# Optimization experiments

Measured on AMD Instinct MI355X. Metric: run time of the kernel, lower is better.

The kernel has to match this reference:

```python
import jax, jax.numpy as jnp
import numpy as np

N = 100000   # num_nodes
E = 1600000  # num_edges
DIN = 128
H1 = 256
H2 = 128
SLOPE = 0.01  # torch leaky_relu default negative slope


def _gcn_conv(h, W, b, src, dst):
    # GCNConv: add self-loops, symmetric deg^-1/2 normalization, linear transform, scatter-add, bias
    hw = h @ W  # [N, out]
    loops = jnp.arange(N)
    s = jnp.concatenate([src, loops])
    d = jnp.concatenate([dst, loops])
    deg = jax.ops.segment_sum(jnp.ones(s.shape[0], dtype=hw.dtype), d, num_segments=N)
    dis = jnp.where(deg > 0, jax.lax.rsqrt(deg), 0.0)
    msg = hw[s] * (dis[s] * dis[d])[:, None]
    return jax.ops.segment_sum(msg, d, num_segments=N) + b


def _gru_cell(x, h, Wih, Whh, bih, bhh):
    # torch.nn.GRUCell semantics; weight layout [3H, in], gate order r, z, n
    gi = x @ Wih.T + bih
    gh = h @ Whh.T + bhh
    ir, iz, inn = jnp.split(gi, 3, axis=-1)
    hr, hz, hn = jnp.split(gh, 3, axis=-1)
    r = jax.nn.sigmoid(ir + hr)
    z = jax.nn.sigmoid(iz + hz)
    n = jnp.tanh(inn + r * hn)
    return (1.0 - z) * n + z * h


def setup_inputs() -> dict:
    key = jax.random.key(0)
    ks = jax.random.split(key, 24)
    rn = lambda k, shape, s=0.05: (jax.random.normal(k, shape) * s).astype(jnp.float32)
    return {
        "x": rn(ks[0], (N, DIN), 1.0),
        "edge_index": jax.random.randint(ks[1], (2, E), 0, N, dtype=jnp.int32),
        "prev0": rn(ks[2], (N, H1), 1.0),
        "prev1": rn(ks[3], (N, H2), 1.0),
        "Wp1": rn(ks[4], (DIN, 256)), "bp1": jnp.zeros((256,), jnp.float32),
        "Wp2": rn(ks[5], (256, 128)), "bp2": jnp.zeros((128,), jnp.float32),
        "Wc1": rn(ks[6], (128, H1)), "bc1": jnp.zeros((H1,), jnp.float32),
        "Wc2": rn(ks[7], (H1, H2)), "bc2": jnp.zeros((H2,), jnp.float32),
        "Wih1": rn(ks[8], (3 * H1, H1)), "Whh1": rn(ks[9], (3 * H1, H1)),
        "bih1": jnp.zeros((3 * H1,), jnp.float32), "bhh1": jnp.zeros((3 * H1,), jnp.float32),
        "Wih2": rn(ks[10], (3 * H2, H2)), "Whh2": rn(ks[11], (3 * H2, H2)),
        "bih2": jnp.zeros((3 * H2,), jnp.float32), "bhh2": jnp.zeros((3 * H2,), jnp.float32),
        "Wpost": rn(ks[12], (H2, 2)), "bpost": jnp.zeros((2,), jnp.float32),
    }


def reference(x, edge_index, prev0, prev1, Wp1, bp1, Wp2, bp2, Wc1, bc1, Wc2, bc2,
              Wih1, Whh1, bih1, bhh1, Wih2, Whh2, bih2, bhh2, Wpost, bpost):
    src, dst = edge_index[0], edge_index[1]
    # preprocess MLP (dropout p=0 => identity)
    h = jax.nn.leaky_relu(x @ Wp1 + bp1, SLOPE)
    h = jax.nn.leaky_relu(h @ Wp2 + bp2, SLOPE)
    # GCN layer 1 + GRU temporal update
    h = jax.nn.leaky_relu(_gcn_conv(h, Wc1, bc1, src, dst), SLOPE)
    h = _gru_cell(h, prev0, Wih1, Whh1, bih1, bhh1)
    emb0 = h
    # GCN layer 2 + GRU temporal update
    h = jax.nn.leaky_relu(_gcn_conv(h, Wc2, bc2, src, dst), SLOPE)
    h = _gru_cell(h, prev1, Wih2, Whh2, bih2, bhh2)
    emb1 = h
    # postprocess and reduce
    out = jnp.sum(h @ Wpost + bpost, axis=-1)  # [N]
    return out, emb0, emb1
```

## Files before the change

### kernel.cpp

```cpp
#include <hip/hip_runtime.h>
#include <cstdint>
#include <cstddef>

typedef __bf16 bf16x8 __attribute__((ext_vector_type(8)));
typedef float f32x4 __attribute__((ext_vector_type(4)));
typedef unsigned short us16;

__device__ __forceinline__ float lrelu(float v) { return v >= 0.0f ? v : 0.01f * v; }
__device__ __forceinline__ float fsigmoid(float x) {
  x = fminf(fmaxf(x, -30.0f), 30.0f);
  return 1.0f / (1.0f + __expf(-x));
}
__device__ __forceinline__ float ftanh(float x) {
  x = fminf(fmaxf(x, -15.0f), 15.0f);
  float e = __expf(2.0f * x);
  return (e - 1.0f) / (e + 1.0f);
}
__device__ __forceinline__ us16 f2b(float f) {
  unsigned int u = __builtin_bit_cast(unsigned int, f);
  u = (u + 0x7fffu + ((u >> 16) & 1u)) >> 16;
  return (us16)u;
}
__device__ __forceinline__ float b2f(us16 h) {
  unsigned int u = ((unsigned int)h) << 16;
  return __builtin_bit_cast(float, u);
}
__device__ __forceinline__ unsigned pk2(float a, float b) {
  return (unsigned)f2b(a) | ((unsigned)f2b(b) << 16);
}
__device__ __forceinline__ void unp8(int4 v, float* t) {
  unsigned a = (unsigned)v.x, b = (unsigned)v.y, c = (unsigned)v.z, d = (unsigned)v.w;
  t[0] = b2f((us16)(a & 0xffff)); t[1] = b2f((us16)(a >> 16));
  t[2] = b2f((us16)(b & 0xffff)); t[3] = b2f((us16)(b >> 16));
  t[4] = b2f((us16)(c & 0xffff)); t[5] = b2f((us16)(c >> 16));
  t[6] = b2f((us16)(d & 0xffff)); t[7] = b2f((us16)(d >> 16));
}

__device__ __forceinline__ void stage16(const us16* gsrc, us16* ldst) {
  __builtin_amdgcn_global_load_lds(
      (const __attribute__((address_space(1))) unsigned int*)(const void*)gsrc,
      (__attribute__((address_space(3))) unsigned int*)(void*)ldst, 16, 0, 0);
}
__device__ __forceinline__ bf16x8 frag_rd(const us16* base, int row, int byte_in_row) {
  int byte = row * 128 + (byte_in_row ^ ((row & 7) << 4));
  return *(const bf16x8*)((const char*)base + byte);
}

__global__ void k_deg(const int* __restrict__ dst, int* __restrict__ indeg, int E) {
  int e = blockIdx.x * 256 + threadIdx.x;
  if (e < E) atomicAdd(&indeg[dst[e]], 1);
}

__global__ void k_dis(const int* __restrict__ indeg, float* __restrict__ dis, int n) {
  int i = blockIdx.x * 256 + threadIdx.x;
  if (i < n) dis[i] = rsqrtf((float)(indeg[i] + 1));
}

__global__ __launch_bounds__(1024) void k_scan1(const int* __restrict__ v, int* __restrict__ rp,
                                                int* __restrict__ part, int n) {
  __shared__ int wsum[16];
  int base = blockIdx.x << 10;
  int t = threadIdx.x, lane = t & 63, wv = t >> 6;
  int val = (base + t < n) ? v[base + t] : 0;
  int s = val;
  #pragma unroll
  for (int off = 1; off < 64; off <<= 1) {
    int u = __shfl_up(s, off);
    if (lane >= off) s += u;
  }
  if (lane == 63) wsum[wv] = s;
  __syncthreads();
  int wadd = 0;
  #pragma unroll
  for (int w = 0; w < 16; ++w) wadd += (w < wv) ? wsum[w] : 0;
  if (base + t < n) rp[base + t] = wadd + s - val;
  if (t == 0) {
    int tot = 0;
    #pragma unroll
    for (int w = 0; w < 16; ++w) tot += wsum[w];
    part[blockIdx.x] = tot;
  }
}

__global__ __launch_bounds__(1024) void k_scan2(int* __restrict__ p, int nc) {
  __shared__ int wsum[16];
  int t = threadIdx.x, lane = t & 63, wv = t >> 6;
  int val = (t < nc) ? p[t] : 0;
  int s = val;
  #pragma unroll
  for (int off = 1; off < 64; off <<= 1) {
    int u = __shfl_up(s, off);
    if (lane >= off) s += u;
  }
  if (lane == 63) wsum[wv] = s;
  __syncthreads();
  int wadd = 0;
  #pragma unroll
  for (int w = 0; w < 16; ++w) wadd += (w < wv) ? wsum[w] : 0;
  if (t < nc) p[t] = wadd + s - val;
}

__global__ void k_scan3(int* __restrict__ rp, const int* __restrict__ part, int n, int total) {
  int i = blockIdx.x * 256 + threadIdx.x;
  if (i < n) rp[i] += part[i >> 10];
  else if (i == n) rp[n] = total;
}

__global__ void k_fill(const int* __restrict__ src, const int* __restrict__ dst,
                       const float* __restrict__ dis, int* __restrict__ cursor,
                       int* __restrict__ csrc, float* __restrict__ cw, int E) {
  int e = blockIdx.x * 256 + threadIdx.x;
  if (e >= E) return;
  int s = src[e], d = dst[e];
  int pos = atomicAdd(&cursor[d], 1);
  csrc[pos] = s;
  cw[pos] = dis[s] * dis[d];
}

__global__ void k_cast(const float* __restrict__ in, us16* __restrict__ out, int n) {
  int i = (blockIdx.x * 256 + threadIdx.x) * 4;
  if (i >= n) return;
  float4 v = *(const float4*)(in + i);
  *(ushort4*)(out + i) = make_ushort4(f2b(v.x), f2b(v.y), f2b(v.z), f2b(v.w));
}

__global__ void k_tpose(const float* __restrict__ in, us16* __restrict__ out, int R, int C) {
  int t = blockIdx.x * 256 + threadIdx.x;
  if (t >= R * C) return;
  int r = t % R, c = t / R;
  out[(size_t)c * R + r] = f2b(in[(size_t)r * C + c]);
}

template<int ACT, int BIAS>
__global__ __launch_bounds__(256) void k_mm(const us16* __restrict__ A,
                                            const us16* __restrict__ Bt,
                                            const float* __restrict__ bias,
                                            us16* __restrict__ Cb,
                                            int M, int K, int Nc, int ny) {
  __shared__ __align__(16) us16 As[128 * 64];
  __shared__ __align__(16) us16 Bs[128 * 64];
  const int bm = (blockIdx.x / ny) * 128;
  const int bn = (blockIdx.x % ny) * 128;
  const int tid = threadIdx.x;
  const int lane = tid & 63;
  const int wave = tid >> 6;
  const int wm = (wave >> 1) * 64;
  const int wn = (wave & 1) * 64;
  const int lr = lane & 15;
  const int lk = lane >> 4;
  const int srow = lane >> 3;
  const int schk = (lane & 7) ^ srow;
  f32x4 acc[4][4] = {};
  for (int k0 = 0; k0 < K; k0 += 64) {
    #pragma unroll
    for (int it = 0; it < 4; ++it) {
      int r8 = (wave * 4 + it) * 8;
      int ar = bm + r8 + srow; if (ar >= M) ar = M - 1;
      stage16(A + (size_t)ar * K + k0 + schk * 8, As + r8 * 64);
      stage16(Bt + (size_t)(bn + r8 + srow) * K + k0 + schk * 8, Bs + r8 * 64);
    }
    __syncthreads();
    #pragma unroll
    for (int kk = 0; kk < 2; ++kk) {
      bf16x8 af[4], bq[4];
      #pragma unroll
      for (int i = 0; i < 4; ++i) af[i] = frag_rd(As, wm + i * 16 + lr, kk * 64 + lk * 16);
      #pragma unroll
      for (int j = 0; j < 4; ++j) bq[j] = frag_rd(Bs, wn + j * 16 + lr, kk * 64 + lk * 16);
      #pragma unroll
      for (int i = 0; i < 4; ++i)
        #pragma unroll
        for (int j = 0; j < 4; ++j)
          acc[i][j] = __builtin_amdgcn_mfma_f32_16x16x32_bf16(af[i], bq[j], acc[i][j], 0, 0, 0);
    }
    __syncthreads();
  }
  float bb[4];
  #pragma unroll
  for (int j = 0; j < 4; ++j) bb[j] = BIAS ? bias[bn + wn + j * 16 + lr] : 0.0f;
  #pragma unroll
  for (int i = 0; i < 4; ++i) {
    #pragma unroll
    for (int q = 0; q < 4; ++q) {
      int row = bm + wm + i * 16 + lk * 4 + q;
      if (row < M) {
        #pragma unroll
        for (int j = 0; j < 4; ++j) {
          int col = bn + wn + j * 16 + lr;
          float v = acc[i][j][q] + bb[j];
          if (ACT) v = lrelu(v);
          Cb[(size_t)row * Nc + col] = f2b(v);
        }
      }
    }
  }
}

template<int ACT>
__global__ __launch_bounds__(256) void k_agg128(const us16* __restrict__ hw, const int* __restrict__ rp,
                                                const int* __restrict__ csrc, const float* __restrict__ cw,
                                                const float* __restrict__ dis, const float* __restrict__ bias,
                                                us16* __restrict__ outp, int M) {
  int node = blockIdx.x * 16 + (threadIdx.x >> 4);
  int l = threadIdx.x & 15;
  if (node >= M) return;
  const us16* base = hw + l * 8;
  float acc[8], t0[8], t1[8], t2[8], t3[8];
  float dn = dis[node];
  float sw = dn * dn;
  {
    int4 v = *(const int4*)(base + (size_t)node * 128);
    unp8(v, t0);
    #pragma unroll
    for (int j = 0; j < 8; ++j) acc[j] = t0[j] * sw;
  }
  int e = rp[node], e1 = rp[node + 1];
  for (; e + 4 <= e1; e += 4) {
    int s0 = csrc[e], s1 = csrc[e + 1], s2 = csrc[e + 2], s3 = csrc[e + 3];
    float w0 = cw[e], w1 = cw[e + 1], w2 = cw[e + 2], w3 = cw[e + 3];
    int4 v0 = *(const int4*)(base + (size_t)s0 * 128);
    int4 v1 = *(const int4*)(base + (size_t)s1 * 128);
    int4 v2 = *(const int4*)(base + (size_t)s2 * 128);
    int4 v3 = *(const int4*)(base + (size_t)s3 * 128);
    unp8(v0, t0); unp8(v1, t1); unp8(v2, t2); unp8(v3, t3);
    #pragma unroll
    for (int j = 0; j < 8; ++j) acc[j] = fmaf(w0, t0[j], acc[j]);
    #pragma unroll
    for (int j = 0; j < 8; ++j) acc[j] = fmaf(w1, t1[j], acc[j]);
    #pragma unroll
    for (int j = 0; j < 8; ++j) acc[j] = fmaf(w2, t2[j], acc[j]);
    #pragma unroll
    for (int j = 0; j < 8; ++j) acc[j] = fmaf(w3, t3[j], acc[j]);
  }
  for (; e < e1; ++e) {
    int s0 = csrc[e];
    float w0 = cw[e];
    int4 v0 = *(const int4*)(base + (size_t)s0 * 128);
    unp8(v0, t0);
    #pragma unroll
    for (int j = 0; j < 8; ++j) acc[j] = fmaf(w0, t0[j], acc[j]);
  }
  if (ACT) {
    float4 b0 = *(const float4*)(bias + l * 8);
    float4 b1 = *(const float4*)(bias + l * 8 + 4);
    float bb[8] = {b0.x, b0.y, b0.z, b0.w, b1.x, b1.y, b1.z, b1.w};
    #pragma unroll
    for (int j = 0; j < 8; ++j) acc[j] = lrelu(acc[j] + bb[j]);
  }
  int4 o;
  o.x = (int)pk2(acc[0], acc[1]);
  o.y = (int)pk2(acc[2], acc[3]);
  o.z = (int)pk2(acc[4], acc[5]);
  o.w = (int)pk2(acc[6], acc[7]);
  *(int4*)(outp + (size_t)node * 128 + l * 8) = o;
}

template<int H, int WB>
__global__ __launch_bounds__(256) void k_fgru(const us16* __restrict__ xb, const us16* __restrict__ hb,
                                              const us16* __restrict__ Wih, const us16* __restrict__ Whh,
                                              const float* __restrict__ bih, const float* __restrict__ bhh,
                                              float* __restrict__ emb, us16* __restrict__ embb,
                                              int M, int ny) {
  __shared__ __align__(16) us16 as_[128 * 64];
  __shared__ __align__(16) us16 ws[3 * 64 * 64];
  const int bn = (blockIdx.x % ny) * 64;
  const int bm = (blockIdx.x / ny) * 128;
  const int tid = threadIdx.x;
  const int lane = tid & 63, wave = tid >> 6;
  const int wm = (wave >> 1) * 64, wn = (wave & 1) * 32;
  const int lr = lane & 15, lk = lane >> 4;
  const int srow = lane >> 3;
  const int schk = (lane & 7) ^ srow;

  f32x4 acc[3][4][2];
  #pragma unroll
  for (int g = 0; g < 3; ++g)
    #pragma unroll
    for (int i = 0; i < 4; ++i)
      #pragma unroll
      for (int j = 0; j < 2; ++j) acc[g][i][j] = {0.f, 0.f, 0.f, 0.f};

  for (int k0 = 0; k0 < H; k0 += 64) {
    #pragma unroll
    for (int it = 0; it < 4; ++it) {
      int r8 = (wave * 4 + it) * 8;
      int ar = bm + r8 + srow; if (ar >= M) ar = M - 1;
      stage16(xb + (size_t)ar * H + k0 + schk * 8, as_ + r8 * 64);
    }
    #pragma unroll
    for (int it = 0; it < 6; ++it) {
      int idx = wave * 6 + it;
      int g = idx >> 3, rr = (idx & 7) * 8;
      stage16(Wih + (size_t)(g * H + bn + rr + srow) * H + k0 + schk * 8,
              ws + g * 64 * 64 + rr * 64);
    }
    __syncthreads();
    #pragma unroll
    for (int kk = 0; kk < 2; ++kk) {
      bf16x8 a[4], bq[3][2];
      #pragma unroll
      for (int i = 0; i < 4; ++i) a[i] = frag_rd(as_, wm + i * 16 + lr, kk * 64 + lk * 16);
      #pragma unroll
      for (int g = 0; g < 3; ++g)
        #pragma unroll
        for (int j = 0; j < 2; ++j)
          bq[g][j] = frag_rd(ws + g * 64 * 64, wn + j * 16 + lr, kk * 64 + lk * 16);
      #pragma unroll
      for (int g = 0; g < 3; ++g)
        #pragma unroll
        for (int i = 0; i < 4; ++i)
          #pragma unroll
          for (int j = 0; j < 2; ++j)
            acc[g][i][j] = __builtin_amdgcn_mfma_f32_16x16x32_bf16(a[i], bq[g][j], acc[g][i][j], 0, 0, 0);
    }
    __syncthreads();
  }
  uint2 pgi[3][4][2];
  #pragma unroll
  for (int g = 0; g < 3; ++g)
    #pragma unroll
    for (int i = 0; i < 4; ++i)
      #pragma unroll
      for (int j = 0; j < 2; ++j) {
        pgi[g][i][j].x = pk2(acc[g][i][j][0], acc[g][i][j][1]);
        pgi[g][i][j].y = pk2(acc[g][i][j][2], acc[g][i][j][3]);
        acc[g][i][j] = {0.f, 0.f, 0.f, 0.f};
      }
  for (int k0 = 0; k0 < H; k0 += 64) {
    #pragma unroll
    for (int it = 0; it < 4; ++it) {
      int r8 = (wave * 4 + it) * 8;
      int ar = bm + r8 + srow; if (ar >= M) ar = M - 1;
      stage16(hb + (size_t)ar * H + k0 + schk * 8, as_ + r8 * 64);
    }
    #pragma unroll
    for (int it = 0; it < 6; ++it) {
      int idx = wave * 6 + it;
      int g = idx >> 3, rr = (idx & 7) * 8;
      stage16(Whh + (size_t)(g * H + bn + rr + srow) * H + k0 + schk * 8,
              ws + g * 64 * 64 + rr * 64);
    }
    __syncthreads();
    #pragma unroll
    for (int kk = 0; kk < 2; ++kk) {
      bf16x8 a[4], bq[3][2];
      #pragma unroll
      for (int i = 0; i < 4; ++i) a[i] = frag_rd(as_, wm + i * 16 + lr, kk * 64 + lk * 16);
      #pragma unroll
      for (int g = 0; g < 3; ++g)
        #pragma unroll
        for (int j = 0; j < 2; ++j)
          bq[g][j] = frag_rd(ws + g * 64 * 64, wn + j * 16 + lr, kk * 64 + lk * 16);
      #pragma unroll
      for (int g = 0; g < 3; ++g)
        #pragma unroll
        for (int i = 0; i < 4; ++i)
          #pragma unroll
          for (int j = 0; j < 2; ++j)
            acc[g][i][j] = __builtin_amdgcn_mfma_f32_16x16x32_bf16(a[i], bq[g][j], acc[g][i][j], 0, 0, 0);
    }
    __syncthreads();
  }
  #pragma unroll
  for (int j = 0; j < 2; ++j) {
    int col = bn + wn + j * 16 + lr;
    float sr = bih[col] + bhh[col];
    float sz = bih[H + col] + bhh[H + col];
    float bni = bih[2 * H + col];
    float bnh = bhh[2 * H + col];
    #pragma unroll
    for (int i = 0; i < 4; ++i) {
      #pragma unroll
      for (int q = 0; q < 4; ++q) {
        int row = bm + wm + i * 16 + lk * 4 + q;
        if (row >= M) continue;
        unsigned w0 = (q & 2) ? pgi[0][i][j].y : pgi[0][i][j].x;
        unsigned w1 = (q & 2) ? pgi[1][i][j].y : pgi[1][i][j].x;
        unsigned w2 = (q & 2) ? pgi[2][i][j].y : pgi[2][i][j].x;
        int sh = (q & 1) * 16;
        float gir = b2f((us16)(w0 >> sh));
        float giz = b2f((us16)(w1 >> sh));
        float gin = b2f((us16)(w2 >> sh));
        float r = fsigmoid(gir + acc[0][i][j][q] + sr);
        float z = fsigmoid(giz + acc[1][i][j][q] + sz);
        float n = ftanh(gin + bni + r * (acc[2][i][j][q] + bnh));
        float hv = b2f(hb[(size_t)row * H + col]);
        float o = (1.0f - z) * n + z * hv;
        emb[(size_t)row * H + col] = o;
        if (WB) embb[(size_t)row * H + col] = f2b(o);
      }
    }
  }
}

__global__ __launch_bounds__(256) void k_post(const float* __restrict__ emb, const float* __restrict__ Wpost,
                                              const float* __restrict__ bpost, float* __restrict__ outv, int M) {
  int gw = (int)((blockIdx.x * 256 + threadIdx.x) >> 6);
  int lane = threadIdx.x & 63;
  if (gw >= M) return;
  float2 ev = *(const float2*)(emb + (size_t)gw * 128 + lane * 2);
  float4 wv = *(const float4*)(Wpost + lane * 4);
  float p = ev.x * (wv.x + wv.y) + ev.y * (wv.z + wv.w);
  #pragma unroll
  for (int o = 32; o > 0; o >>= 1) p += __shfl_xor(p, o);
  if (lane == 0) outv[gw] = p + bpost[0] + bpost[1];
}

extern "C" void kernel_launch(void* const* d_in, const int* in_sizes, int n_in,
                              void* d_out, int out_size, void* d_ws, size_t ws_size,
                              hipStream_t stream) {
  const float* x     = (const float*)d_in[0];
  const int*   ei    = (const int*)d_in[1];
  const float* prev0 = (const float*)d_in[2];
  const float* prev1 = (const float*)d_in[3];
  const float* Wp1   = (const float*)d_in[4];
  const float* bp1   = (const float*)d_in[5];
  const float* Wp2   = (const float*)d_in[6];
  const float* bp2   = (const float*)d_in[7];
  const float* Wc1   = (const float*)d_in[8];
  const float* bc1   = (const float*)d_in[9];
  const float* Wc2   = (const float*)d_in[10];
  const float* bc2   = (const float*)d_in[11];
  const float* Wih1  = (const float*)d_in[12];
  const float* Whh1  = (const float*)d_in[13];
  const float* bih1  = (const float*)d_in[14];
  const float* bhh1  = (const float*)d_in[15];
  const float* Wih2  = (const float*)d_in[16];
  const float* Whh2  = (const float*)d_in[17];
  const float* bih2  = (const float*)d_in[18];
  const float* bhh2  = (const float*)d_in[19];
  const float* Wpost = (const float*)d_in[20];
  const float* bpost = (const float*)d_in[21];

  const int N = in_sizes[0] / 128;
  const int E = in_sizes[1] / 2;
  const int* srcp = ei;
  const int* dstp = ei + E;

  char* wsb = (char*)d_ws;
  size_t off = 0;
  auto alloc = [&](size_t bytes) -> void* {
    void* p = wsb + off;
    off = (off + bytes + 255) & ~(size_t)255;
    return p;
  };
  float* dis    = (float*)alloc((size_t)N * 4);
  int*   indeg  = (int*)alloc((size_t)N * 4);
  int*   rp     = (int*)alloc((size_t)(N + 1) * 4);
  int*   part   = (int*)alloc((size_t)1024 * 4);
  int*   cursor = (int*)alloc((size_t)N * 4);
  int*   csrc   = (int*)alloc((size_t)E * 4);
  float* cw     = (float*)alloc((size_t)E * 4);
  us16* xb    = (us16*)alloc((size_t)N * 128 * 2);
  us16* p0b   = (us16*)alloc((size_t)N * 256 * 2);
  us16* p1b   = (us16*)alloc((size_t)N * 128 * 2);
  us16* WtP1  = (us16*)alloc((size_t)256 * 128 * 2);
  us16* WtP2  = (us16*)alloc((size_t)128 * 256 * 2);
  us16* WtC1  = (us16*)alloc((size_t)256 * 128 * 2);
  us16* WtC2  = (us16*)alloc((size_t)128 * 256 * 2);
  us16* Wih1b = (us16*)alloc((size_t)768 * 256 * 2);
  us16* Whh1b = (us16*)alloc((size_t)768 * 256 * 2);
  us16* Wih2b = (us16*)alloc((size_t)384 * 128 * 2);
  us16* Whh2b = (us16*)alloc((size_t)384 * 128 * 2);
  us16* bufA  = (us16*)alloc((size_t)N * 256 * 2);
  us16* bufB  = (us16*)alloc((size_t)N * 128 * 2);
  us16* bufD  = (us16*)alloc((size_t)N * 128 * 2);
  us16* emb0b = (us16*)alloc((size_t)N * 256 * 2);
  (void)ws_size; (void)n_in; (void)out_size;

  float* outv = (float*)d_out;
  float* emb0 = outv + N;
  float* emb1 = emb0 + (size_t)N * 256;

  auto cg = [](long n) { return (unsigned)((n / 4 + 255) / 256); };

  k_cast<<<cg((long)N * 128), 256, 0, stream>>>(x, xb, N * 128);
  k_cast<<<cg((long)N * 256), 256, 0, stream>>>(prev0, p0b, N * 256);
  k_cast<<<cg((long)N * 128), 256, 0, stream>>>(prev1, p1b, N * 128);
  k_cast<<<cg(768 * 256), 256, 0, stream>>>(Wih1, Wih1b, 768 * 256);
  k_cast<<<cg(768 * 256), 256, 0, stream>>>(Whh1, Whh1b, 768 * 256);
  k_cast<<<cg(384 * 128), 256, 0, stream>>>(Wih2, Wih2b, 384 * 128);
  k_cast<<<cg(384 * 128), 256, 0, stream>>>(Whh2, Whh2b, 384 * 128);
  k_tpose<<<(128 * 256 + 255) / 256, 256, 0, stream>>>(Wp1, WtP1, 128, 256);
  k_tpose<<<(256 * 128 + 255) / 256, 256, 0, stream>>>(Wp2, WtP2, 256, 128);
  k_tpose<<<(128 * 256 + 255) / 256, 256, 0, stream>>>(Wc1, WtC1, 128, 256);
  k_tpose<<<(256 * 128 + 255) / 256, 256, 0, stream>>>(Wc2, WtC2, 256, 128);

  hipMemsetAsync(indeg, 0, (size_t)N * 4, stream);
  k_deg<<<(E + 255) / 256, 256, 0, stream>>>(dstp, indeg, E);
  k_dis<<<(N + 255) / 256, 256, 0, stream>>>(indeg, dis, N);
  const int NC = (N + 1023) / 1024;
  k_scan1<<<NC, 1024, 0, stream>>>(indeg, rp, part, N);
  k_scan2<<<1, 1024, 0, stream>>>(part, NC);
  k_scan3<<<(N + 256) / 256, 256, 0, stream>>>(rp, part, N, E);
  hipMemcpyAsync(cursor, rp, (size_t)N * 4, hipMemcpyDeviceToDevice, stream);
  k_fill<<<(E + 255) / 256, 256, 0, stream>>>(srcp, dstp, dis, cursor, csrc, cw, E);

  const int MB = (N + 127) / 128;
  const int AB = (N + 15) / 16;

  k_mm<1, 1><<<MB * 2, 256, 0, stream>>>(xb, WtP1, bp1, bufA, N, 128, 256, 2);
  k_mm<1, 1><<<MB, 256, 0, stream>>>(bufA, WtP2, bp2, bufB, N, 256, 128, 1);
  k_agg128<0><<<AB, 256, 0, stream>>>(bufB, rp, csrc, cw, dis, nullptr, bufD, N);
  k_mm<1, 1><<<MB * 2, 256, 0, stream>>>(bufD, WtC1, bc1, bufA, N, 128, 256, 2);
  k_fgru<256, 1><<<MB * 4, 256, 0, stream>>>(bufA, p0b, Wih1b, Whh1b, bih1, bhh1,
                                             emb0, emb0b, N, 4);
  k_mm<0, 0><<<MB, 256, 0, stream>>>(emb0b, WtC2, nullptr, bufB, N, 256, 128, 1);
  k_agg128<1><<<AB, 256, 0, stream>>>(bufB, rp, csrc, cw, dis, bc2, bufD, N);
  k_fgru<128, 0><<<MB * 2, 256, 0, stream>>>(bufD, p1b, Wih2b, Whh2b, bih2, bhh2,
                                             emb1, nullptr, N, 2);
  k_post<<<(N + 3) / 4, 256, 0, stream>>>(emb1, Wpost, bpost, outv, N);
}
```

Baseline: 896.7 us.

## Double-buffer LDS in GEMM and fuse GRU input/hidden GEMMs into one pipelined loop

The matmul kernel now double-buffers its LDS tiles, so the next K-slice is staged while MFMAs run on the current one, and one barrier per step is dropped. The GRU kernel is restructured to compute the input and hidden gate GEMMs together in a single K loop over 32-wide slices. It uses a 64-row tile, its own double-buffered staging and a new swizzle, and keeps six fp32 accumulator sets instead of packing the input-gate results to bf16. This removes the serial second pass, the bf16 round-trip of gi and the exposed load latency. In exchange it doubles LDS use and launches more, smaller blocks, which may cost occupancy.

```diff
diff --git a/kernel.cpp b/kernel.cpp
--- a/kernel.cpp
+++ b/kernel.cpp
@@ -44,6 +44,10 @@
 __device__ __forceinline__ bf16x8 frag_rd(const us16* base, int row, int byte_in_row) {
   int byte = row * 128 + (byte_in_row ^ ((row & 7) << 4));
   return *(const bf16x8*)((const char*)base + byte);
+}
+__device__ __forceinline__ bf16x8 frd32(const us16* tilebase, int row, int ck16) {
+  int slot = ck16 ^ ((row >> 1) & 3);
+  return *(const bf16x8*)(tilebase + row * 32 + slot * 8);
 }
 
 __global__ void k_deg(const int* __restrict__ dst, int* __restrict__ indeg, int E) {
@@ -137,8 +141,7 @@
                                             const float* __restrict__ bias,
                                             us16* __restrict__ Cb,
                                             int M, int K, int Nc, int ny) {
-  __shared__ __align__(16) us16 As[128 * 64];
-  __shared__ __align__(16) us16 Bs[128 * 64];
+  __shared__ __align__(16) us16 lds[2][2 * 8192];
   const int bm = (blockIdx.x / ny) * 128;
   const int bn = (blockIdx.x % ny) * 128;
   const int tid = threadIdx.x;
@@ -151,29 +154,36 @@
   const int srow = lane >> 3;
   const int schk = (lane & 7) ^ srow;
   f32x4 acc[4][4] = {};
-  for (int k0 = 0; k0 < K; k0 += 64) {
+
+  auto stage = [&](int k0, us16* buf) {
     #pragma unroll
     for (int it = 0; it < 4; ++it) {
       int r8 = (wave * 4 + it) * 8;
       int ar = bm + r8 + srow; if (ar >= M) ar = M - 1;
-      stage16(A + (size_t)ar * K + k0 + schk * 8, As + r8 * 64);
-      stage16(Bt + (size_t)(bn + r8 + srow) * K + k0 + schk * 8, Bs + r8 * 64);
-    }
+      stage16(A + (size_t)ar * K + k0 + schk * 8, buf + r8 * 64);
+      stage16(Bt + (size_t)(bn + r8 + srow) * K + k0 + schk * 8, buf + 8192 + r8 * 64);
+    }
+  };
+
+  const int nk = K >> 6;
+  stage(0, lds[0]);
+  for (int t = 0; t < nk; ++t) {
+    us16* cur = lds[t & 1];
     __syncthreads();
+    if (t + 1 < nk) stage((t + 1) << 6, lds[(t + 1) & 1]);
     #pragma unroll
     for (int kk = 0; kk < 2; ++kk) {
       bf16x8 af[4], bq[4];
       #pragma unroll
-      for (int i = 0; i < 4; ++i) af[i] = frag_rd(As, wm + i * 16 + lr, kk * 64 + lk * 16);
-      #pragma unroll
-      for (int j = 0; j < 4; ++j) bq[j] = frag_rd(Bs, wn + j * 16 + lr, kk * 64 + lk * 16);
+      for (int i = 0; i < 4; ++i) af[i] = frag_rd(cur, wm + i * 16 + lr, kk * 64 + lk * 16);
+      #pragma unroll
+      for (int j = 0; j < 4; ++j) bq[j] = frag_rd(cur + 8192, wn + j * 16 + lr, kk * 64 + lk * 16);
       #pragma unroll
       for (int i = 0; i < 4; ++i)
         #pragma unroll
         for (int j = 0; j < 4; ++j)
           acc[i][j] = __builtin_amdgcn_mfma_f32_16x16x32_bf16(af[i], bq[j], acc[i][j], 0, 0, 0);
     }
-    __syncthreads();
   }
   float bb[4];
   #pragma unroll
@@ -261,129 +271,91 @@
                                               const float* __restrict__ bih, const float* __restrict__ bhh,
                                               float* __restrict__ emb, us16* __restrict__ embb,
                                               int M, int ny) {
-  __shared__ __align__(16) us16 as_[128 * 64];
-  __shared__ __align__(16) us16 ws[3 * 64 * 64];
+  __shared__ __align__(16) us16 lds[2][8 * 2048];
   const int bn = (blockIdx.x % ny) * 64;
-  const int bm = (blockIdx.x / ny) * 128;
+  const int bm = (blockIdx.x / ny) * 64;
   const int tid = threadIdx.x;
   const int lane = tid & 63, wave = tid >> 6;
-  const int wm = (wave >> 1) * 64, wn = (wave & 1) * 32;
+  const int wm = (wave >> 1) * 32, wn = (wave & 1) * 32;
   const int lr = lane & 15, lk = lane >> 4;
-  const int srow = lane >> 3;
-  const int schk = (lane & 7) ^ srow;
-
-  f32x4 acc[3][4][2];
-  #pragma unroll
-  for (int g = 0; g < 3; ++g)
-    #pragma unroll
-    for (int i = 0; i < 4; ++i)
+  const int sl_row = lane >> 2;
+  const int sl_chk = (lane & 3) ^ ((lane >> 3) & 3);
+
+  f32x4 acc[6][2][2];
+  #pragma unroll
+  for (int g = 0; g < 6; ++g)
+    #pragma unroll
+    for (int i = 0; i < 2; ++i)
       #pragma unroll
       for (int j = 0; j < 2; ++j) acc[g][i][j] = {0.f, 0.f, 0.f, 0.f};
 
-  for (int k0 = 0; k0 < H; k0 += 64) {
-    #pragma unroll
-    for (int it = 0; it < 4; ++it) {
-      int r8 = (wave * 4 + it) * 8;
-      int ar = bm + r8 + srow; if (ar >= M) ar = M - 1;
-      stage16(xb + (size_t)ar * H + k0 + schk * 8, as_ + r8 * 64);
-    }
-    #pragma unroll
-    for (int it = 0; it < 6; ++it) {
-      int idx = wave * 6 + it;
-      int g = idx >> 3, rr = (idx & 7) * 8;
-      stage16(Wih + (size_t)(g * H + bn + rr + srow) * H + k0 + schk * 8,
-              ws + g * 64 * 64 + rr * 64);
-    }
+  auto stage_step = [&](int k0, us16* buf) {
+    #pragma unroll
+    for (int it = 0; it < 8; ++it) {
+      int m = wave * 8 + it;
+      int t = m >> 2, q = m & 3;
+      int r0 = q * 16;
+      int lrow = r0 + sl_row;
+      const us16* src;
+      if (t == 0) {
+        int ar = bm + lrow; if (ar >= M) ar = M - 1;
+        src = xb + (size_t)ar * H + k0 + sl_chk * 8;
+      } else if (t == 1) {
+        int ar = bm + lrow; if (ar >= M) ar = M - 1;
+        src = hb + (size_t)ar * H + k0 + sl_chk * 8;
+      } else {
+        int w = t - 2;
+        const us16* W = (w < 3) ? Wih : Whh;
+        int g = (w < 3) ? w : w - 3;
+        src = W + (size_t)(g * H + bn + lrow) * H + k0 + sl_chk * 8;
+      }
+      stage16(src, buf + t * 2048 + r0 * 32);
+    }
+  };
+
+  const int nk = H >> 5;
+  stage_step(0, lds[0]);
+  for (int t = 0; t < nk; ++t) {
+    us16* cur = lds[t & 1];
     __syncthreads();
-    #pragma unroll
-    for (int kk = 0; kk < 2; ++kk) {
-      bf16x8 a[4], bq[3][2];
-      #pragma unroll
-      for (int i = 0; i < 4; ++i) a[i] = frag_rd(as_, wm + i * 16 + lr, kk * 64 + lk * 16);
-      #pragma unroll
-      for (int g = 0; g < 3; ++g)
+    if (t + 1 < nk) stage_step((t + 1) << 5, lds[(t + 1) & 1]);
+    bf16x8 ax[2], ah[2];
+    #pragma unroll
+    for (int i = 0; i < 2; ++i) {
+      ax[i] = frd32(cur, wm + i * 16 + lr, lk);
+      ah[i] = frd32(cur + 2048, wm + i * 16 + lr, lk);
+    }
+    #pragma unroll
+    for (int g = 0; g < 3; ++g) {
+      bf16x8 bqi[2], bqh[2];
+      #pragma unroll
+      for (int j = 0; j < 2; ++j) {
+        bqi[j] = frd32(cur + (2 + g) * 2048, wn + j * 16 + lr, lk);
+        bqh[j] = frd32(cur + (5 + g) * 2048, wn + j * 16 + lr, lk);
+      }
+      #pragma unroll
+      for (int i = 0; i < 2; ++i)
         #pragma unroll
-        for (int j = 0; j < 2; ++j)
-          bq[g][j] = frag_rd(ws + g * 64 * 64, wn + j * 16 + lr, kk * 64 + lk * 16);
-      #pragma unroll
-      for (int g = 0; g < 3; ++g)
-        #pragma unroll
-        for (int i = 0; i < 4; ++i)
-          #pragma unroll
-          for (int j = 0; j < 2; ++j)
-            acc[g][i][j] = __builtin_amdgcn_mfma_f32_16x16x32_bf16(a[i], bq[g][j], acc[g][i][j], 0, 0, 0);
-    }
-    __syncthreads();
-  }
-  uint2 pgi[3][4][2];
-  #pragma unroll
-  for (int g = 0; g < 3; ++g)
-    #pragma unroll
-    for (int i = 0; i < 4; ++i)
-      #pragma unroll
-      for (int j = 0; j < 2; ++j) {
-        pgi[g][i][j].x = pk2(acc[g][i][j][0], acc[g][i][j][1]);
-        pgi[g][i][j].y = pk2(acc[g][i][j][2], acc[g][i][j][3]);
-        acc[g][i][j] = {0.f, 0.f, 0.f, 0.f};
-      }
-  for (int k0 = 0; k0 < H; k0 += 64) {
-    #pragma unroll
-    for (int it = 0; it < 4; ++it) {
-      int r8 = (wave * 4 + it) * 8;
-      int ar = bm + r8 + srow; if (ar >= M) ar = M - 1;
-      stage16(hb + (size_t)ar * H + k0 + schk * 8, as_ + r8 * 64);
-    }
-    #pragma unroll
-    for (int it = 0; it < 6; ++it) {
-      int idx = wave * 6 + it;
-      int g = idx >> 3, rr = (idx & 7) * 8;
-      stage16(Whh + (size_t)(g * H + bn + rr + srow) * H + k0 + schk * 8,
-              ws + g * 64 * 64 + rr * 64);
-    }
-    __syncthreads();
-    #pragma unroll
-    for (int kk = 0; kk < 2; ++kk) {
-      bf16x8 a[4], bq[3][2];
-      #pragma unroll
-      for (int i = 0; i < 4; ++i) a[i] = frag_rd(as_, wm + i * 16 + lr, kk * 64 + lk * 16);
-      #pragma unroll
-      for (int g = 0; g < 3; ++g)
-        #pragma unroll
-        for (int j = 0; j < 2; ++j)
-          bq[g][j] = frag_rd(ws + g * 64 * 64, wn + j * 16 + lr, kk * 64 + lk * 16);
-      #pragma unroll
-      for (int g = 0; g < 3; ++g)
-        #pragma unroll
-        for (int i = 0; i < 4; ++i)
-          #pragma unroll
-          for (int j = 0; j < 2; ++j)
-            acc[g][i][j] = __builtin_amdgcn_mfma_f32_16x16x32_bf16(a[i], bq[g][j], acc[g][i][j], 0, 0, 0);
-    }
-    __syncthreads();
+        for (int j = 0; j < 2; ++j) {
+          acc[g][i][j] = __builtin_amdgcn_mfma_f32_16x16x32_bf16(ax[i], bqi[j], acc[g][i][j], 0, 0, 0);
+          acc[3 + g][i][j] = __builtin_amdgcn_mfma_f32_16x16x32_bf16(ah[i], bqh[j], acc[3 + g][i][j], 0, 0, 0);
+        }
+    }
   }
   #pragma unroll
   for (int j = 0; j < 2; ++j) {
     int col = bn + wn + j * 16 + lr;
-    float sr = bih[col] + bhh[col];
-    float sz = bih[H + col] + bhh[H + col];
-    float bni = bih[2 * H + col];
-    float bnh = bhh[2 * H + col];
-    #pragma unroll
-    for (int i = 0; i < 4; ++i) {
+    float bir = bih[col], biz = bih[H + col], bin = bih[2 * H + col];
+    float bhr = bhh[col], bhz = bhh[H + col], bhn = bhh[2 * H + col];
+    #pragma unroll
+    for (int i = 0; i < 2; ++i) {
       #pragma unroll
       for (int q = 0; q < 4; ++q) {
         int row = bm + wm + i * 16 + lk * 4 + q;
         if (row >= M) continue;
-        unsigned w0 = (q & 2) ? pgi[0][i][j].y : pgi[0][i][j].x;
-        unsigned w1 = (q & 2) ? pgi[1][i][j].y : pgi[1][i][j].x;
-        unsigned w2 = (q & 2) ? pgi[2][i][j].y : pgi[2][i][j].x;
-        int sh = (q & 1) * 16;
-        float gir = b2f((us16)(w0 >> sh));
-        float giz = b2f((us16)(w1 >> sh));
-        float gin = b2f((us16)(w2 >> sh));
-        float r = fsigmoid(gir + acc[0][i][j][q] + sr);
-        float z = fsigmoid(giz + acc[1][i][j][q] + sz);
-        float n = ftanh(gin + bni + r * (acc[2][i][j][q] + bnh));
+        float r = fsigmoid(acc[0][i][j][q] + bir + acc[3][i][j][q] + bhr);
+        float z = fsigmoid(acc[1][i][j][q] + biz + acc[4][i][j][q] + bhz);
+        float n = ftanh(acc[2][i][j][q] + bin + r * (acc[5][i][j][q] + bhn));
         float hv = b2f(hb[(size_t)row * H + col]);
         float o = (1.0f - z) * n + z * hv;
         emb[(size_t)row * H + col] = o;
@@ -497,17 +469,18 @@
   k_fill<<<(E + 255) / 256, 256, 0, stream>>>(srcp, dstp, dis, cursor, csrc, cw, E);
 
   const int MB = (N + 127) / 128;
+  const int FB = (N + 63) / 64;
   const int AB = (N + 15) / 16;
 
   k_mm<1, 1><<<MB * 2, 256, 0, stream>>>(xb, WtP1, bp1, bufA, N, 128, 256, 2);
   k_mm<1, 1><<<MB, 256, 0, stream>>>(bufA, WtP2, bp2, bufB, N, 256, 128, 1);
   k_agg128<0><<<AB, 256, 0, stream>>>(bufB, rp, csrc, cw, dis, nullptr, bufD, N);
   k_mm<1, 1><<<MB * 2, 256, 0, stream>>>(bufD, WtC1, bc1, bufA, N, 128, 256, 2);
-  k_fgru<256, 1><<<MB * 4, 256, 0, stream>>>(bufA, p0b, Wih1b, Whh1b, bih1, bhh1,
+  k_fgru<256, 1><<<FB * 4, 256, 0, stream>>>(bufA, p0b, Wih1b, Whh1b, bih1, bhh1,
                                              emb0, emb0b, N, 4);
   k_mm<0, 0><<<MB, 256, 0, stream>>>(emb0b, WtC2, nullptr, bufB, N, 256, 128, 1);
   k_agg128<1><<<AB, 256, 0, stream>>>(bufB, rp, csrc, cw, dis, bc2, bufD, N);
-  k_fgru<128, 0><<<MB * 2, 256, 0, stream>>>(bufD, p1b, Wih2b, Whh2b, bih2, bhh2,
+  k_fgru<128, 0><<<FB * 2, 256, 0, stream>>>(bufD, p1b, Wih2b, Whh2b, bih2, bhh2,
                                              emb1, nullptr, N, 2);
   k_post<<<(N + 3) / 4, 256, 0, stream>>>(emb1, Wpost, bpost, outv, N);
 }
```

Measured after the change: 799.9 us. -10.8%, faster.
